# Performance work log

Hardware: AMD Instinct MI355X
Metric: run time of the kernel (lower is better)

Reference implementation:

```python
import jax, jax.numpy as jnp
import numpy as np

NHEAD = 16


def corrcoef(X, Y):
    # X, Y: [..., S, D]; Pearson correlation between rows of X and rows of Y
    X = X - X.mean(-1, keepdims=True)
    Y = Y - Y.mean(-1, keepdims=True)
    c = jnp.einsum('...id,...jd->...ij', X, Y)            # [..., S, S]
    d = jnp.einsum('...id,...id->...i', X, Y)             # diagonal of c
    stddev = jnp.sqrt(d)
    c = c / stddev[..., :, None]
    c = c / stddev[..., None, :]
    c = jnp.clip(c, -1.0, 1.0)
    return jnp.where(jnp.isnan(c), 0.0, c)


def setup_inputs() -> dict:
    key = jax.random.key(0)
    k1, k2, k3 = jax.random.split(key, 3)
    T, B, D = 2048, 2, 1024
    query = jax.random.normal(k1, (T, B, D), dtype=jnp.float32)
    W_qkv = jax.random.normal(k2, (3 * D, D), dtype=jnp.float32) * (1.0 / np.sqrt(D))
    b_qkv = jax.random.normal(k3, (3 * D,), dtype=jnp.float32) * 0.01
    return {"query": query, "W_qkv": W_qkv, "b_qkv": b_qkv}


def reference(query, W_qkv, b_qkv):
    T, B, D = query.shape
    hd = D // NHEAD
    qkv = query @ W_qkv.T + b_qkv                          # [T, B, 3D]
    q, k, v = jnp.split(qkv, 3, axis=-1)

    def to_bhsd(x):
        return x.reshape(T, B, NHEAD, hd).transpose(1, 2, 0, 3)  # [B, H, S, hd]

    q, k, v = to_bhsd(q), to_bhsd(k), to_bhsd(v)
    corr = corrcoef(q, k)                                   # [B, H, S, S]
    corr = jax.nn.softmax(corr, axis=-1)                    # eval: dropout_p = 0
    return corr @ v                                         # [B, H, S, hd]
```

## Files before the change

### kernel.cpp

```cpp
#include <hip/hip_runtime.h>

#define S 2048
#define D 1024
#define NH 16
#define HD 64
#define N3 3072
#define M 4096

typedef short s16x8 __attribute__((ext_vector_type(8)));
typedef _Float16 f16x8 __attribute__((ext_vector_type(8)));
typedef float f32x4 __attribute__((ext_vector_type(4)));
typedef float f32x16 __attribute__((ext_vector_type(16)));
typedef unsigned int u32;
typedef u32 u32x4 __attribute__((ext_vector_type(4)));

#define LOG2E 1.44269504088896340736f

__device__ __forceinline__ unsigned short f2bf(float f) {
  unsigned u = __builtin_bit_cast(unsigned, f);
  u += 0x7fffu + ((u >> 16) & 1u);
  return (unsigned short)(u >> 16);
}
__device__ __forceinline__ float bf2f(unsigned short h) {
  return __builtin_bit_cast(float, (unsigned)h << 16);
}
__device__ __forceinline__ unsigned short f2h(float f) {
  _Float16 h = (_Float16)f;
  return __builtin_bit_cast(unsigned short, h);
}

__device__ __forceinline__ float wsum(float v) {
  #pragma unroll
  for (int m = 1; m < 64; m <<= 1) v += __shfl_xor(v, m, 64);
  return v;
}

__device__ __forceinline__ void gload_lds16(const unsigned short* g, unsigned short* l) {
  __builtin_amdgcn_global_load_lds(
      (const __attribute__((address_space(1))) u32*)g,
      (__attribute__((address_space(3))) u32*)l, 16, 0, 0);
}
__device__ __forceinline__ void gload_lds4(const float* g, float* l) {
  __builtin_amdgcn_global_load_lds(
      (const __attribute__((address_space(1))) u32*)g,
      (__attribute__((address_space(3))) u32*)l, 4, 0, 0);
}

__global__ __launch_bounds__(256) void split_k(const float* __restrict__ q,
                                               const float* __restrict__ w,
                                               unsigned short* __restrict__ A1,
                                               unsigned short* __restrict__ A2,
                                               unsigned short* __restrict__ W1,
                                               unsigned short* __restrict__ W2) {
  const size_t gid = (size_t)blockIdx.x * 256 + threadIdx.x;
  const size_t NA = (size_t)M * D / 4;
  float4 x;
  unsigned short* p1; unsigned short* p2; size_t qi; float scale;
  if (gid < NA) {
    qi = gid;  x = ((const float4*)q)[qi];
    p1 = A1; p2 = A2; scale = 64.f;
  } else {
    qi = gid - NA;  x = ((const float4*)w)[qi];
    p1 = W1; p2 = W2; scale = 1024.f;
  }
  float e[4] = {x.x * scale, x.y * scale, x.z * scale, x.w * scale};
  unsigned short h1[4], h2[4];
  #pragma unroll
  for (int i = 0; i < 4; ++i) {
    _Float16 a = (_Float16)e[i];
    float r = e[i] - (float)a;
    _Float16 b = (_Float16)r;
    h1[i] = __builtin_bit_cast(unsigned short, a);
    h2[i] = __builtin_bit_cast(unsigned short, b);
  }
  *(ushort4*)&p1[qi * 4] = make_ushort4(h1[0], h1[1], h1[2], h1[3]);
  *(ushort4*)&p2[qi * 4] = make_ushort4(h2[0], h2[1], h2[2], h2[3]);
}

__global__ __launch_bounds__(256) void gemm_mfma(const unsigned short* __restrict__ A1,
                                                 const unsigned short* __restrict__ A2,
                                                 const unsigned short* __restrict__ W1,
                                                 const unsigned short* __restrict__ W2,
                                                 const float* __restrict__ bias,
                                                 float* __restrict__ C) {
  __shared__ unsigned short As[128 * 64];
  __shared__ unsigned short Bs[128 * 64];
  const int tid = threadIdx.x;
  const int w = tid >> 6, l = tid & 63;
  const int lo = l & 15, hi = l >> 4;
  const int n0 = blockIdx.x * 128, m0 = blockIdx.y * 128;
  const int wr = w >> 1, wc = w & 1;

  const int nseg = (n0 >= 2048) ? 1 : 3;

  const int srow = (tid >> 3) & 31;
  const int skc = tid & 7;

  f32x4 acc[4][4];
  #pragma unroll
  for (int mi = 0; mi < 4; ++mi)
    #pragma unroll
    for (int nj = 0; nj < 4; ++nj) acc[mi][nj] = (f32x4){0.f, 0.f, 0.f, 0.f};

  for (int s = 0; s < 3; ++s) {
    if (s >= nseg) break;
    const unsigned short* Ab;
    const unsigned short* Bb;
    switch (s) {
      case 0: Ab = A1; Bb = W1; break;
      case 1: Ab = A2; Bb = W1; break;
      default: Ab = A1; Bb = W2; break;
    }
    Ab += (size_t)m0 * D;
    Bb += (size_t)n0 * D;

    for (int k0 = 0; k0 < D; k0 += 64) {
      __syncthreads();
      #pragma unroll
      for (int c = 0; c < 4; ++c) {
        const int row = c * 32 + srow;
        const int koct = skc ^ (row & 7);
        gload_lds16(Ab + (size_t)row * D + k0 + koct * 8,
                    As + c * 2048 + w * 512);
        gload_lds16(Bb + (size_t)row * D + k0 + koct * 8,
                    Bs + c * 2048 + w * 512);
      }
      __syncthreads();

      f16x8 af[4][2], bf[4][2];
      #pragma unroll
      for (int mi = 0; mi < 4; ++mi)
        #pragma unroll
        for (int ks = 0; ks < 2; ++ks) {
          const int row = wr * 64 + mi * 16 + lo;
          const int koct = (ks * 4 + hi) ^ (lo & 7);
          af[mi][ks] = *(const f16x8*)&As[row * 64 + koct * 8];
        }
      #pragma unroll
      for (int nj = 0; nj < 4; ++nj)
        #pragma unroll
        for (int ks = 0; ks < 2; ++ks) {
          const int row = wc * 64 + nj * 16 + lo;
          const int koct = (ks * 4 + hi) ^ (lo & 7);
          bf[nj][ks] = *(const f16x8*)&Bs[row * 64 + koct * 8];
        }
      #pragma unroll
      for (int mi = 0; mi < 4; ++mi)
        #pragma unroll
        for (int nj = 0; nj < 4; ++nj)
          #pragma unroll
          for (int ks = 0; ks < 2; ++ks)
            acc[mi][nj] = __builtin_amdgcn_mfma_f32_16x16x32_f16(
                af[mi][ks], bf[nj][ks], acc[mi][nj], 0, 0, 0);
    }
  }

  #pragma unroll
  for (int mi = 0; mi < 4; ++mi)
    #pragma unroll
    for (int nj = 0; nj < 4; ++nj) {
      const int n = n0 + wc * 64 + nj * 16 + lo;
      const float bj = bias[n];
      #pragma unroll
      for (int r = 0; r < 4; ++r) {
        const int m = m0 + wr * 64 + mi * 16 + hi * 4 + r;
        C[(size_t)m * N3 + n] = acc[mi][nj][r] * (1.f / 65536.f) + bj;
      }
    }
}

__global__ __launch_bounds__(256) void stats_k(const float* __restrict__ qkv,
                                               unsigned short* __restrict__ qhi,
                                               unsigned short* __restrict__ qlo,
                                               unsigned short* __restrict__ khi,
                                               unsigned short* __restrict__ klo,
                                               unsigned short* __restrict__ vt,
                                               float* __restrict__ rs) {
  __shared__ unsigned short VsT[64][65];
  const int tt = blockIdx.x, bh = blockIdx.y;
  const int b = bh >> 4, h = bh & 15;
  const int w = threadIdx.x >> 6, l = threadIdx.x & 63;

  for (int rr = 0; rr < 16; ++rr) {
    const int t = tt * 64 + w * 16 + rr;
    const size_t base = (size_t)(t * 2 + b) * N3 + h * HD;
    const float q = qkv[base + l];
    const float k = qkv[base + D + l];
    const float v = qkv[base + 2 * D + l];
    const float qm = wsum(q) * (1.f / 64.f);
    const float km = wsum(k) * (1.f / 64.f);
    const float qcv = q - qm, kcv = k - km;
    const float d = wsum(qcv * kcv);
    float rv = 0.f;
    if (d > 0.f) {
      rv = rsqrtf(d);
      rv = rv * (1.5f - 0.5f * d * rv * rv);
      rv *= 1.20112240872f;
    }
    const size_t ro = ((size_t)bh * S + t) * HD + l;
    const unsigned short qh = f2bf(qcv);
    const unsigned short kh = f2bf(kcv);
    qhi[ro] = qh;  qlo[ro] = f2bf(qcv - bf2f(qh));
    khi[ro] = kh;  klo[ro] = f2bf(kcv - bf2f(kh));
    if (l == 0) rs[(size_t)bh * S + t] = rv;
    VsT[l][w * 16 + rr] = f2h(v);
  }
  __syncthreads();
  const int dd = threadIdx.x >> 2, seg = threadIdx.x & 3;
  unsigned pk[8];
  #pragma unroll
  for (int e = 0; e < 8; ++e) {
    unsigned l2 = VsT[dd][seg * 16 + 2 * e];
    unsigned h2 = VsT[dd][seg * 16 + 2 * e + 1];
    pk[e] = l2 | (h2 << 16);
  }
  unsigned short* dst = vt + ((size_t)bh * HD + dd) * S + tt * 64 + seg * 16;
  *(uint4*)dst       = make_uint4(pk[0], pk[1], pk[2], pk[3]);
  *(uint4*)(dst + 8) = make_uint4(pk[4], pk[5], pk[6], pk[7]);
}

__global__ __launch_bounds__(256) void attn_k(const unsigned short* __restrict__ qhi,
                                              const unsigned short* __restrict__ qlo,
                                              const unsigned short* __restrict__ khi,
                                              const unsigned short* __restrict__ klo,
                                              const unsigned short* __restrict__ vt,
                                              const float* __restrict__ rs,
                                              float* __restrict__ out) {
  __shared__ unsigned short Kh[2 * 4096];
  __shared__ unsigned short Kl[2 * 4096];
  __shared__ unsigned short Vsm[2 * 4096];
  __shared__ float Rsl[2 * 64];

  const int tid = threadIdx.x;
  const int w = tid >> 6, l = tid & 63;
  const int lq = l & 31;
  const int h = l >> 5;
  const int l7 = l & 7;

  const int wgid = blockIdx.x;
  const int orig = (wgid & 7) * 64 + (wgid >> 3);
  const int bh = orig >> 4, qt = orig & 15;

  const unsigned short* qhb = qhi + (size_t)bh * S * HD;
  const unsigned short* qlb = qlo + (size_t)bh * S * HD;
  const unsigned short* khb = khi + (size_t)bh * S * HD;
  const unsigned short* klb = klo + (size_t)bh * S * HD;
  const unsigned short* vbase = vt + (size_t)bh * HD * S;
  const float* rbase = rs + (size_t)bh * S;
  const int qrow0 = qt * 128 + w * 32;

  const int srow3 = l >> 3;
  const int sg = l7 ^ srow3;

  s16x8 qfh[4], qfl[4];
  #pragma unroll
  for (int kc = 0; kc < 4; ++kc) {
    const size_t off = (size_t)(qrow0 + lq) * HD + kc * 16 + h * 8;
    qfh[kc] = *(const s16x8*)(qhb + off);
    qfl[kc] = *(const s16x8*)(qlb + off);
  }
  const float rsq = rbase[qrow0 + lq];

  f32x16 oacc[2];
  oacc[0] = (f32x16)(0.f);
  oacc[1] = (f32x16)(0.f);
  float den = 0.f;

  auto STAGE = [&](int buf, int j0) {
    #pragma unroll
    for (int c = 0; c < 2; ++c) {
      const int row = c * 32 + w * 8 + srow3;
      const int dst = buf * 4096 + c * 2048 + w * 512;
      gload_lds16(khb + (size_t)(j0 + row) * HD + sg * 8, Kh + dst);
      gload_lds16(klb + (size_t)(j0 + row) * HD + sg * 8, Kl + dst);
      gload_lds16(vbase + (size_t)row * S + j0 + sg * 8, Vsm + dst);
    }
    if (w == 0) gload_lds4(rbase + j0 + l, Rsl + buf * 64);
  };

  STAGE(0, 0);
  __syncthreads();

  int cur = 0;
  for (int t = 0; t < 32; ++t) {
    if (t < 31) STAGE(cur ^ 1, (t + 1) * 64);

    const int cb = cur * 4096;
    #pragma unroll
    for (int jblk = 0; jblk < 2; ++jblk) {
      f32x16 sacc = (f32x16)(0.f);
      #pragma unroll
      for (int kc = 0; kc < 4; ++kc) {
        const int off = cb + (jblk * 32 + lq) * 64 + (((kc * 2 + h) ^ l7) << 3);
        s16x8 akh = *(const s16x8*)&Kh[off];
        s16x8 akl = *(const s16x8*)&Kl[off];
        sacc = __builtin_amdgcn_mfma_f32_32x32x16_bf16(akh, qfh[kc], sacc, 0, 0, 0);
        sacc = __builtin_amdgcn_mfma_f32_32x32x16_bf16(akl, qfh[kc], sacc, 0, 0, 0);
        sacc = __builtin_amdgcn_mfma_f32_32x32x16_bf16(akh, qfl[kc], sacc, 0, 0, 0);
      }

      u32 pkA[4], pkB[4];
      #pragma unroll
      for (int g = 0; g < 4; ++g) {
        f32x4 rjv = *(const f32x4*)&Rsl[cur * 64 + jblk * 32 + g * 8 + h * 4];
        float e0, e1, e2, e3;
        {
          float t0 = fminf(LOG2E, fmaxf(-LOG2E, sacc[4 * g + 0] * rsq * rjv[0]));
          float t1 = fminf(LOG2E, fmaxf(-LOG2E, sacc[4 * g + 1] * rsq * rjv[1]));
          float t2 = fminf(LOG2E, fmaxf(-LOG2E, sacc[4 * g + 2] * rsq * rjv[2]));
          float t3 = fminf(LOG2E, fmaxf(-LOG2E, sacc[4 * g + 3] * rsq * rjv[3]));
          e0 = exp2f(t0); e1 = exp2f(t1); e2 = exp2f(t2); e3 = exp2f(t3);
        }
        den += (e0 + e1) + (e2 + e3);
        pkA[g] = __builtin_bit_cast(u32, __builtin_amdgcn_cvt_pkrtz(e0, e1));
        pkB[g] = __builtin_bit_cast(u32, __builtin_amdgcn_cvt_pkrtz(e2, e3));
      }

      #pragma unroll
      for (int jc2 = 0; jc2 < 2; ++jc2) {
        const u32 sA = h ? pkA[2 * jc2] : pkA[2 * jc2 + 1];
        const u32 sB = h ? pkB[2 * jc2] : pkB[2 * jc2 + 1];
        const u32 rA = (u32)__shfl_xor((int)sA, 32, 64);
        const u32 rB = (u32)__shfl_xor((int)sB, 32, 64);
        u32x4 uu;
        uu[0] = h ? rA : pkA[2 * jc2];
        uu[1] = h ? rB : pkB[2 * jc2];
        uu[2] = h ? pkA[2 * jc2 + 1] : rA;
        uu[3] = h ? pkB[2 * jc2 + 1] : rB;
        const f16x8 pa = __builtin_bit_cast(f16x8, uu);

        const int jcg = jblk * 2 + jc2;
        #pragma unroll
        for (int dblk = 0; dblk < 2; ++dblk) {
          const int voff = cb + (dblk * 32 + lq) * 64 + (((jcg * 2 + h) ^ l7) << 3);
          f16x8 bv = *(const f16x8*)&Vsm[voff];
          oacc[dblk] = __builtin_amdgcn_mfma_f32_32x32x16_f16(pa, bv, oacc[dblk], 0, 0, 0);
        }
      }
    }

    __syncthreads();
    cur ^= 1;
  }

  const float dtot = den + __shfl_xor(den, 32, 64);
  const float inv = 1.f / dtot;

  #pragma unroll
  for (int g = 0; g < 4; ++g)
    #pragma unroll
    for (int i = 0; i < 4; ++i) {
      const int qr = i + 8 * g + 4 * h;
      const float invq = __shfl(inv, i + 8 * g + 4 * h, 64);
      const size_t row = (size_t)bh * S + qrow0 + qr;
      out[row * HD + lq]      = oacc[0][4 * g + i] * invq;
      out[row * HD + 32 + lq] = oacc[1][4 * g + i] * invq;
    }
}

extern "C" void kernel_launch(void* const* d_in, const int* in_sizes, int n_in,
                              void* d_out, int out_size, void* d_ws, size_t ws_size,
                              hipStream_t stream) {
  const float* query = (const float*)d_in[0];
  const float* W     = (const float*)d_in[1];
  const float* bias  = (const float*)d_in[2];
  float* out = (float*)d_out;
  char* ws = (char*)d_ws;

  float*          qkv = (float*)ws;
  unsigned short* A1 = (unsigned short*)(ws + 50331648);
  unsigned short* A2 = (unsigned short*)(ws + 58720256);
  unsigned short* W1 = (unsigned short*)(ws + 67108864);
  unsigned short* W2 = (unsigned short*)(ws + 73400320);
  unsigned short* qhi = (unsigned short*)(ws + 50331648);
  unsigned short* qlo = (unsigned short*)(ws + 58720256);
  unsigned short* khi = (unsigned short*)(ws + 67108864);
  unsigned short* klo = (unsigned short*)(ws + 75497472);
  unsigned short* vt  = (unsigned short*)(ws + 83886080);
  float*          rsb = (float*)(ws + 92274688);

  split_k  <<<dim3(7168), 256, 0, stream>>>(query, W, A1, A2, W1, W2);
  gemm_mfma<<<dim3(24, 32), 256, 0, stream>>>(A1, A2, W1, W2, bias, qkv);
  stats_k  <<<dim3(32, 32), 256, 0, stream>>>(qkv, qhi, qlo, khi, klo, vt, rsb);
  attn_k   <<<dim3(512), 256, 0, stream>>>(qhi, qlo, khi, klo, vt, rsb, out);
}
```

Before: 193.0 us.

## Split attention key range across two wave groups and combine partials in LDS

The attention kernel now launches 512 threads per block: two groups of four waves each process half of the key sequence for the same 128 query rows. Each group accumulates a partial output and denominator, and the second group's partials are reduced through shared memory before the output is written. The double-buffered prefetch is replaced by a single-buffered load guarded by two barriers per iteration. This doubles the resident waves per query tile to raise occupancy and latency hiding on 512 blocks, at the cost of losing load/compute overlap within a group and adding a final LDS reduction.

After: 217.4 us. 1.13x slower.

```diff
diff --git a/kernel.cpp b/kernel.cpp
--- a/kernel.cpp
+++ b/kernel.cpp
@@ -219,23 +219,24 @@
   *(uint4*)(dst + 8) = make_uint4(pk[4], pk[5], pk[6], pk[7]);
 }
 
-__global__ __launch_bounds__(256) void attn_k(const unsigned short* __restrict__ qhi,
-                                              const unsigned short* __restrict__ qlo,
-                                              const unsigned short* __restrict__ khi,
-                                              const unsigned short* __restrict__ klo,
-                                              const unsigned short* __restrict__ vt,
-                                              const float* __restrict__ rs,
-                                              float* __restrict__ out) {
-  __shared__ unsigned short Kh[2 * 4096];
-  __shared__ unsigned short Kl[2 * 4096];
-  __shared__ unsigned short Vsm[2 * 4096];
-  __shared__ float Rsl[2 * 64];
+__global__ __launch_bounds__(512, 4) void attn_k(const unsigned short* __restrict__ qhi,
+                                                 const unsigned short* __restrict__ qlo,
+                                                 const unsigned short* __restrict__ khi,
+                                                 const unsigned short* __restrict__ klo,
+                                                 const unsigned short* __restrict__ vt,
+                                                 const float* __restrict__ rs,
+                                                 float* __restrict__ out) {
+  __shared__ __align__(16) char smem[49664];
+  unsigned short* Kh = (unsigned short*)smem;
+  unsigned short* Kl = (unsigned short*)(smem + 16384);
+  unsigned short* Vs = (unsigned short*)(smem + 32768);
+  float* Rsl = (float*)(smem + 49152);
 
   const int tid = threadIdx.x;
   const int w = tid >> 6, l = tid & 63;
-  const int lq = l & 31;
-  const int h = l >> 5;
-  const int l7 = l & 7;
+  const int wq = w & 3;
+  const int wh = w >> 2;
+  const int lq = l & 31, h = l >> 5, l7 = l & 7;
 
   const int wgid = blockIdx.x;
   const int orig = (wgid & 7) * 64 + (wgid >> 3);
@@ -247,7 +248,7 @@
   const unsigned short* klb = klo + (size_t)bh * S * HD;
   const unsigned short* vbase = vt + (size_t)bh * HD * S;
   const float* rbase = rs + (size_t)bh * S;
-  const int qrow0 = qt * 128 + w * 32;
+  const int qrow0 = qt * 128 + wq * 32;
 
   const int srow3 = l >> 3;
   const int sg = l7 ^ srow3;
@@ -266,32 +267,29 @@
   oacc[1] = (f32x16)(0.f);
   float den = 0.f;
 
-  auto STAGE = [&](int buf, int j0) {
+  const int hb = wh * 4096;
+  const int jbeg = wh * 1024;
+
+  for (int t = 0; t < 16; ++t) {
+    const int j0 = jbeg + t * 64;
+    __syncthreads();
     #pragma unroll
     for (int c = 0; c < 2; ++c) {
-      const int row = c * 32 + w * 8 + srow3;
-      const int dst = buf * 4096 + c * 2048 + w * 512;
+      const int row = c * 32 + wq * 8 + srow3;
+      const int dst = hb + c * 2048 + wq * 512;
       gload_lds16(khb + (size_t)(j0 + row) * HD + sg * 8, Kh + dst);
       gload_lds16(klb + (size_t)(j0 + row) * HD + sg * 8, Kl + dst);
-      gload_lds16(vbase + (size_t)row * S + j0 + sg * 8, Vsm + dst);
-    }
-    if (w == 0) gload_lds4(rbase + j0 + l, Rsl + buf * 64);
-  };
-
-  STAGE(0, 0);
-  __syncthreads();
-
-  int cur = 0;
-  for (int t = 0; t < 32; ++t) {
-    if (t < 31) STAGE(cur ^ 1, (t + 1) * 64);
-
-    const int cb = cur * 4096;
+      gload_lds16(vbase + (size_t)row * S + j0 + sg * 8, Vs + dst);
+    }
+    if (wq == 0) gload_lds4(rbase + j0 + l, Rsl + wh * 64);
+    __syncthreads();
+
     #pragma unroll
     for (int jblk = 0; jblk < 2; ++jblk) {
       f32x16 sacc = (f32x16)(0.f);
       #pragma unroll
       for (int kc = 0; kc < 4; ++kc) {
-        const int off = cb + (jblk * 32 + lq) * 64 + (((kc * 2 + h) ^ l7) << 3);
+        const int off = hb + (jblk * 32 + lq) * 64 + (((kc * 2 + h) ^ l7) << 3);
         s16x8 akh = *(const s16x8*)&Kh[off];
         s16x8 akl = *(const s16x8*)&Kl[off];
         sacc = __builtin_amdgcn_mfma_f32_32x32x16_bf16(akh, qfh[kc], sacc, 0, 0, 0);
@@ -302,7 +300,7 @@
       u32 pkA[4], pkB[4];
       #pragma unroll
       for (int g = 0; g < 4; ++g) {
-        f32x4 rjv = *(const f32x4*)&Rsl[cur * 64 + jblk * 32 + g * 8 + h * 4];
+        f32x4 rjv = *(const f32x4*)&Rsl[wh * 64 + jblk * 32 + g * 8 + h * 4];
         float e0, e1, e2, e3;
         {
           float t0 = fminf(LOG2E, fmaxf(-LOG2E, sacc[4 * g + 0] * rsq * rjv[0]));
@@ -332,30 +330,49 @@
         const int jcg = jblk * 2 + jc2;
         #pragma unroll
         for (int dblk = 0; dblk < 2; ++dblk) {
-          const int voff = cb + (dblk * 32 + lq) * 64 + (((jcg * 2 + h) ^ l7) << 3);
-          f16x8 bv = *(const f16x8*)&Vsm[voff];
+          const int voff = hb + (dblk * 32 + lq) * 64 + (((jcg * 2 + h) ^ l7) << 3);
+          f16x8 bv = *(const f16x8*)&Vs[voff];
           oacc[dblk] = __builtin_amdgcn_mfma_f32_32x32x16_f16(pa, bv, oacc[dblk], 0, 0, 0);
         }
       }
     }
-
-    __syncthreads();
-    cur ^= 1;
-  }
-
-  const float dtot = den + __shfl_xor(den, 32, 64);
-  const float inv = 1.f / dtot;
-
-  #pragma unroll
-  for (int g = 0; g < 4; ++g)
-    #pragma unroll
-    for (int i = 0; i < 4; ++i) {
-      const int qr = i + 8 * g + 4 * h;
-      const float invq = __shfl(inv, i + 8 * g + 4 * h, 64);
-      const size_t row = (size_t)bh * S + qrow0 + qr;
-      out[row * HD + lq]      = oacc[0][4 * g + i] * invq;
-      out[row * HD + 32 + lq] = oacc[1][4 * g + i] * invq;
-    }
+  }
+
+  const float dhalf = den + __shfl_xor(den, 32, 64);
+
+  __syncthreads();
+  float* csum = (float*)smem;
+  float* cden = (float*)(smem + 33792);
+  if (wh == 1) {
+    const int base = (wq * 64 + l) * 33;
+    #pragma unroll
+    for (int r = 0; r < 16; ++r) {
+      csum[base + r]      = oacc[0][r];
+      csum[base + 16 + r] = oacc[1][r];
+    }
+    if (l < 32) cden[wq * 32 + lq] = dhalf;
+  }
+  __syncthreads();
+  if (wh == 0) {
+    const float dtot = dhalf + cden[wq * 32 + lq];
+    const float inv = 1.f / dtot;
+    const int base = (wq * 64 + l) * 33;
+    #pragma unroll
+    for (int r = 0; r < 16; ++r) {
+      oacc[0][r] += csum[base + r];
+      oacc[1][r] += csum[base + 16 + r];
+    }
+    #pragma unroll
+    for (int g = 0; g < 4; ++g)
+      #pragma unroll
+      for (int i = 0; i < 4; ++i) {
+        const int qr = i + 8 * g + 4 * h;
+        const float invq = __shfl(inv, i + 8 * g + 4 * h, 64);
+        const size_t row = (size_t)bh * S + qrow0 + qr;
+        out[row * HD + lq]      = oacc[0][4 * g + i] * invq;
+        out[row * HD + 32 + lq] = oacc[1][4 * g + i] * invq;
+      }
+  }
 }
 
 extern "C" void kernel_launch(void* const* d_in, const int* in_sizes, int n_in,
@@ -382,5 +399,5 @@
   split_k  <<<dim3(7168), 256, 0, stream>>>(query, W, A1, A2, W1, W2);
   gemm_mfma<<<dim3(24, 32), 256, 0, stream>>>(A1, A2, W1, W2, bias, qkv);
   stats_k  <<<dim3(32, 32), 256, 0, stream>>>(qkv, qhi, qlo, khi, klo, vt, rsb);
-  attn_k   <<<dim3(512), 256, 0, stream>>>(qhi, qlo, khi, klo, vt, rsb, out);
-}
+  attn_k   <<<dim3(512), 512, 0, stream>>>(qhi, qlo, khi, klo, vt, rsb, out);
+}
```

## Prefetch two K/V tiles ahead with explicit vmcnt waits and raised priority

Applied to the files above, without the earlier changes.

The attention loop now issues the first two tile loads up front, and each iteration prefetches the tile two steps ahead instead of one. It uses explicit s_waitcnt vmcnt counts and raw s_barrier calls instead of __syncthreads, so global-to-LDS loads stay in flight across barriers. MFMA/softmax compute runs at raised wave priority. The log2e prescale moves out of rsqrt into __expf, and all waves now load the row-scale slice. The gain depends on the hand-counted vmcnt value matching the real number of outstanding loads, which is fragile.

New measurement: 185.9 us. 3.7% less time.

```diff
diff --git a/kernel.cpp b/kernel.cpp
--- a/kernel.cpp
+++ b/kernel.cpp
@@ -13,8 +13,6 @@
 typedef float f32x16 __attribute__((ext_vector_type(16)));
 typedef unsigned int u32;
 typedef u32 u32x4 __attribute__((ext_vector_type(4)));
-
-#define LOG2E 1.44269504088896340736f
 
 __device__ __forceinline__ unsigned short f2bf(float f) {
   unsigned u = __builtin_bit_cast(unsigned, f);
@@ -195,7 +193,6 @@
     if (d > 0.f) {
       rv = rsqrtf(d);
       rv = rv * (1.5f - 0.5f * d * rv * rv);
-      rv *= 1.20112240872f;
     }
     const size_t ro = ((size_t)bh * S + t) * HD + l;
     const unsigned short qh = f2bf(qcv);
@@ -275,17 +272,22 @@
       gload_lds16(klb + (size_t)(j0 + row) * HD + sg * 8, Kl + dst);
       gload_lds16(vbase + (size_t)row * S + j0 + sg * 8, Vsm + dst);
     }
-    if (w == 0) gload_lds4(rbase + j0 + l, Rsl + buf * 64);
+    gload_lds4(rbase + j0 + l, Rsl + buf * 64);
   };
 
   STAGE(0, 0);
-  __syncthreads();
-
-  int cur = 0;
+  STAGE(1, 64);
+
   for (int t = 0; t < 32; ++t) {
-    if (t < 31) STAGE(cur ^ 1, (t + 1) * 64);
-
+    if (t < 31) asm volatile("s_waitcnt vmcnt(7)" ::: "memory");
+    else        asm volatile("s_waitcnt vmcnt(0)" ::: "memory");
+    __builtin_amdgcn_s_barrier();
+    __builtin_amdgcn_sched_barrier(0);
+
+    const int cur = t & 1;
     const int cb = cur * 4096;
+
+    __builtin_amdgcn_s_setprio(1);
     #pragma unroll
     for (int jblk = 0; jblk < 2; ++jblk) {
       f32x16 sacc = (f32x16)(0.f);
@@ -305,11 +307,11 @@
         f32x4 rjv = *(const f32x4*)&Rsl[cur * 64 + jblk * 32 + g * 8 + h * 4];
         float e0, e1, e2, e3;
         {
-          float t0 = fminf(LOG2E, fmaxf(-LOG2E, sacc[4 * g + 0] * rsq * rjv[0]));
-          float t1 = fminf(LOG2E, fmaxf(-LOG2E, sacc[4 * g + 1] * rsq * rjv[1]));
-          float t2 = fminf(LOG2E, fmaxf(-LOG2E, sacc[4 * g + 2] * rsq * rjv[2]));
-          float t3 = fminf(LOG2E, fmaxf(-LOG2E, sacc[4 * g + 3] * rsq * rjv[3]));
-          e0 = exp2f(t0); e1 = exp2f(t1); e2 = exp2f(t2); e3 = exp2f(t3);
+          float c0 = fminf(1.f, fmaxf(-1.f, sacc[4 * g + 0] * rsq * rjv[0]));
+          float c1 = fminf(1.f, fmaxf(-1.f, sacc[4 * g + 1] * rsq * rjv[1]));
+          float c2 = fminf(1.f, fmaxf(-1.f, sacc[4 * g + 2] * rsq * rjv[2]));
+          float c3 = fminf(1.f, fmaxf(-1.f, sacc[4 * g + 3] * rsq * rjv[3]));
+          e0 = __expf(c0); e1 = __expf(c1); e2 = __expf(c2); e3 = __expf(c3);
         }
         den += (e0 + e1) + (e2 + e3);
         pkA[g] = __builtin_bit_cast(u32, __builtin_amdgcn_cvt_pkrtz(e0, e1));
@@ -338,9 +340,12 @@
         }
       }
     }
-
-    __syncthreads();
-    cur ^= 1;
+    __builtin_amdgcn_s_setprio(0);
+
+    __builtin_amdgcn_sched_barrier(0);
+    __builtin_amdgcn_s_barrier();
+    __builtin_amdgcn_sched_barrier(0);
+    if (t + 2 < 32) STAGE(cur, (t + 2) * 64);
   }
 
   const float dtot = den + __shfl_xor(den, 32, 64);
```
